# Performance work log

Hardware: AMD Instinct MI355X
Metric: run time of the kernel (lower is better)

The kernel has to match this reference:

```python
import jax, jax.numpy as jnp
import numpy as np

TAU = 1.0  # initial_temperature, non-trainable
EPS = 1e-10


def setup_inputs() -> dict:
    key = jax.random.key(0)
    ks = jax.random.split(key, 5)
    B, D, E, A = 8192, 1024, 32, 128
    x = jax.random.normal(ks[0], (B, D), dtype=jnp.float32)
    W_att = jax.random.normal(ks[1], (E, D), dtype=jnp.float32) * (1.0 / np.sqrt(D))
    b_att = jnp.zeros((E,), dtype=jnp.float32)
    adaptive_bias = jnp.zeros((E,), dtype=jnp.float32)
    W_strat = jax.random.normal(ks[2], (E, A, D), dtype=jnp.float32) * (1.0 / np.sqrt(D))
    b_strat = jnp.zeros((E, A), dtype=jnp.float32)
    gumbel_u = jax.random.uniform(ks[3], (B, E), dtype=jnp.float32)
    return {"x": x, "W_att": W_att, "b_att": b_att, "adaptive_bias": adaptive_bias,
            "W_strat": W_strat, "b_strat": b_strat, "gumbel_u": gumbel_u}


def reference(x, W_att, b_att, adaptive_bias, W_strat, b_strat, gumbel_u):
    # Gating: linear + adaptive bias, then gumbel-softmax with temperature TAU
    logits = x @ W_att.T + b_att + adaptive_bias            # [B, E]
    g = -jnp.log(-jnp.log(gumbel_u + EPS) + EPS)            # gumbel noise [B, E]
    weights = jax.nn.softmax((logits + g) / TAU, axis=-1)   # [B, E] soft selection
    # Per-strategy outputs: each strategy is Linear(D -> A)
    strat_out = jnp.einsum('bd,ead->bea', x, W_strat) + b_strat  # [B, E, A]
    # Weighted combine (superposition)
    out = jnp.einsum('be,bea->ba', weights, strat_out)      # [B, A]
    return out
```

## Files before the change

kernel.cpp:

```cpp
#include <hip/hip_runtime.h>
#include <stdint.h>

typedef unsigned short u16;
typedef __attribute__((ext_vector_type(4))) float f32x4;
typedef __attribute__((ext_vector_type(8))) short short8;
typedef __attribute__((ext_vector_type(8))) unsigned short u16x8;

static constexpr int Bq = 8192;
static constexpr int Dq = 1024;
static constexpr int Eq = 32;
static constexpr int Aq = 128;
static constexpr int NSTRAT = 4096;

__device__ inline u16 f32_to_bf16_rne(float f) {
    uint32_t u = __float_as_uint(f);
    uint32_t r = 0x7fffu + ((u >> 16) & 1u);
    return (u16)((u + r) >> 16);
}
__device__ inline float bf16_to_f32(u16 h) {
    return __uint_as_float(((uint32_t)h) << 16);
}
__device__ inline void gload_lds16(const u16* g, u16* l) {
    __builtin_amdgcn_global_load_lds(
        (const __attribute__((address_space(1))) void*)g,
        (__attribute__((address_space(3))) void*)l, 16, 0, 0);
}

__global__ __launch_bounds__(256) void cvt_x_kernel(const float* __restrict__ src,
                                                    u16* __restrict__ dst) {
    size_t i = ((size_t)blockIdx.x * 256 + threadIdx.x) * 8;
    f32x4 a = *(const f32x4*)(src + i);
    f32x4 b = *(const f32x4*)(src + i + 4);
    u16x8 o;
    o[0] = f32_to_bf16_rne(a[0]); o[1] = f32_to_bf16_rne(a[1]);
    o[2] = f32_to_bf16_rne(a[2]); o[3] = f32_to_bf16_rne(a[3]);
    o[4] = f32_to_bf16_rne(b[0]); o[5] = f32_to_bf16_rne(b[1]);
    o[6] = f32_to_bf16_rne(b[2]); o[7] = f32_to_bf16_rne(b[3]);
    *(u16x8*)(dst + i) = o;
}

__global__ __launch_bounds__(256) void cvt_w_kernel(const float* __restrict__ src,
                                                    u16* __restrict__ dst) {
    size_t i = ((size_t)blockIdx.x * 256 + threadIdx.x) * 8;
    f32x4 a = *(const f32x4*)(src + i);
    f32x4 b = *(const f32x4*)(src + i + 4);
    u16x8 o;
    o[0] = f32_to_bf16_rne(a[0]); o[1] = f32_to_bf16_rne(a[1]);
    o[2] = f32_to_bf16_rne(a[2]); o[3] = f32_to_bf16_rne(a[3]);
    o[4] = f32_to_bf16_rne(b[0]); o[5] = f32_to_bf16_rne(b[1]);
    o[6] = f32_to_bf16_rne(b[2]); o[7] = f32_to_bf16_rne(b[3]);
    *(u16x8*)(dst + i) = o;
}

#define FBAR do { asm volatile("" ::: "memory"); __builtin_amdgcn_s_barrier(); asm volatile("" ::: "memory"); } while (0)
#define LGKM0 asm volatile("s_waitcnt lgkmcnt(0)" ::: "memory")
#define VMCNT(n) asm volatile("s_waitcnt vmcnt(" #n ")" ::: "memory")
#define SB __builtin_amdgcn_sched_barrier(0)
#define PRIO1 __builtin_amdgcn_s_setprio(1)
#define PRIO0 __builtin_amdgcn_s_setprio(0)
#define MF(a, b, c) __builtin_amdgcn_mfma_f32_16x16x32_bf16(a, b, c, 0, 0, 0)


#define STAGE_A(buf, h, kt) do { \
    gload_lds16(agA + (size_t)((h)*128) * 1024 + (size_t)(kt) * 64, (u16*)&lds[buf][h][tid * 8]); \
    gload_lds16(agA + (size_t)((h)*128 + 64) * 1024 + (size_t)(kt) * 64, (u16*)&lds[buf][h][4096 + tid * 8]); \
} while (0)
#define STAGE_B(buf, h, kt) do { \
    gload_lds16(agB + (size_t)((h)*128) * 1024 + (size_t)(kt) * 64, (u16*)&lds[buf][2 + (h)][tid * 8]); \
    gload_lds16(agB + (size_t)((h)*128 + 64) * 1024 + (size_t)(kt) * 64, (u16*)&lds[buf][2 + (h)][4096 + tid * 8]); \
} while (0)

#define LDA8(DST, ABASE, mq) do { \
    DST[0] = *(const short8*)((ABASE) + (mq)*4096 + 0*1024 + aoff0); \
    DST[1] = *(const short8*)((ABASE) + (mq)*4096 + 0*1024 + aoff1); \
    DST[2] = *(const short8*)((ABASE) + (mq)*4096 + 1*1024 + aoff0); \
    DST[3] = *(const short8*)((ABASE) + (mq)*4096 + 1*1024 + aoff1); \
    DST[4] = *(const short8*)((ABASE) + (mq)*4096 + 2*1024 + aoff0); \
    DST[5] = *(const short8*)((ABASE) + (mq)*4096 + 2*1024 + aoff1); \
    DST[6] = *(const short8*)((ABASE) + (mq)*4096 + 3*1024 + aoff0); \
    DST[7] = *(const short8*)((ABASE) + (mq)*4096 + 3*1024 + aoff1); \
} while (0)
#define LDB4(DST, BBASE, nq) do { \
    DST[0] = *(const short8*)((BBASE) + (nq)*2048 + 0*1024 + boff0); \
    DST[1] = *(const short8*)((BBASE) + (nq)*2048 + 0*1024 + boff1); \
    DST[2] = *(const short8*)((BBASE) + (nq)*2048 + 1*1024 + boff0); \
    DST[3] = *(const short8*)((BBASE) + (nq)*2048 + 1*1024 + boff1); \
} while (0)

#define QUAD(mq, nq, AS, BS) do { \
    acc[(mq)*4+0][(nq)*2+0] = MF(AS[0], BS[0], acc[(mq)*4+0][(nq)*2+0]); \
    acc[(mq)*4+0][(nq)*2+1] = MF(AS[0], BS[2], acc[(mq)*4+0][(nq)*2+1]); \
    acc[(mq)*4+1][(nq)*2+0] = MF(AS[2], BS[0], acc[(mq)*4+1][(nq)*2+0]); \
    acc[(mq)*4+1][(nq)*2+1] = MF(AS[2], BS[2], acc[(mq)*4+1][(nq)*2+1]); \
    acc[(mq)*4+2][(nq)*2+0] = MF(AS[4], BS[0], acc[(mq)*4+2][(nq)*2+0]); \
    acc[(mq)*4+2][(nq)*2+1] = MF(AS[4], BS[2], acc[(mq)*4+2][(nq)*2+1]); \
    acc[(mq)*4+3][(nq)*2+0] = MF(AS[6], BS[0], acc[(mq)*4+3][(nq)*2+0]); \
    acc[(mq)*4+3][(nq)*2+1] = MF(AS[6], BS[2], acc[(mq)*4+3][(nq)*2+1]); \
    acc[(mq)*4+0][(nq)*2+0] = MF(AS[1], BS[1], acc[(mq)*4+0][(nq)*2+0]); \
    acc[(mq)*4+0][(nq)*2+1] = MF(AS[1], BS[3], acc[(mq)*4+0][(nq)*2+1]); \
    acc[(mq)*4+1][(nq)*2+0] = MF(AS[3], BS[1], acc[(mq)*4+1][(nq)*2+0]); \
    acc[(mq)*4+1][(nq)*2+1] = MF(AS[3], BS[3], acc[(mq)*4+1][(nq)*2+1]); \
    acc[(mq)*4+2][(nq)*2+0] = MF(AS[5], BS[1], acc[(mq)*4+2][(nq)*2+0]); \
    acc[(mq)*4+2][(nq)*2+1] = MF(AS[5], BS[3], acc[(mq)*4+2][(nq)*2+1]); \
    acc[(mq)*4+3][(nq)*2+0] = MF(AS[7], BS[1], acc[(mq)*4+3][(nq)*2+0]); \
    acc[(mq)*4+3][(nq)*2+1] = MF(AS[7], BS[3], acc[(mq)*4+3][(nq)*2+1]); \
} while (0)

#define GITER(t, TAIL) do { \
     \
    LDB4(Bs0, Bbase0, 0); \
    STAGE_A(1, 0, (t) + 1); \
    SB; FBAR; LGKM0; SB; \
    PRIO1; QUAD(0, 0, As0, Bs0); PRIO0; SB; FBAR; \
     \
    LDB4(Bs1, Bbase0, 1); \
    STAGE_A(1, 1, (t) + 1); \
    SB; FBAR; LGKM0; SB; \
    PRIO1; QUAD(0, 1, As0, Bs1); PRIO0; SB; FBAR; \
     \
    LDA8(As1, Abase0, 1); \
    if (!(TAIL)) STAGE_B(0, 0, (t) + 2); \
    SB; FBAR; LGKM0; SB; \
    PRIO1; QUAD(1, 1, As1, Bs1); PRIO0; SB; \
    if (TAIL) { VMCNT(0); } else { VMCNT(2); } \
    FBAR; \
     \
    LDA8(As0, Abase1, 0); \
    if (!(TAIL)) STAGE_B(0, 1, (t) + 2); \
    SB; FBAR; LGKM0; SB; \
    PRIO1; QUAD(1, 0, As1, Bs0); PRIO0; SB; FBAR; \
     \
    LDB4(Bs0, Bbase1, 0); \
    if (!(TAIL)) STAGE_A(0, 0, (t) + 2); \
    SB; FBAR; LGKM0; SB; \
    PRIO1; QUAD(0, 0, As0, Bs0); PRIO0; SB; FBAR; \
     \
    LDB4(Bs1, Bbase1, 1); \
    if (!(TAIL)) STAGE_A(0, 1, (t) + 2); \
    SB; FBAR; LGKM0; SB; \
    PRIO1; QUAD(0, 1, As0, Bs1); PRIO0; SB; FBAR; \
     \
    LDA8(As1, Abase1, 1); \
    if (!(TAIL)) STAGE_B(1, 0, (t) + 3); \
    SB; FBAR; LGKM0; SB; \
    PRIO1; QUAD(1, 1, As1, Bs1); PRIO0; SB; \
    if (!(TAIL)) { VMCNT(2); } \
    FBAR; \
     \
    if (!(TAIL)) { LDA8(As0, Abase0, 0); STAGE_B(1, 1, (t) + 3); } \
    SB; FBAR; LGKM0; SB; \
    PRIO1; QUAD(1, 0, As1, Bs0); PRIO0; SB; FBAR; \
} while (0)

__global__ __launch_bounds__(512, 2) void gemm256(const u16* __restrict__ Abuf,
                                                  const u16* __restrict__ Bbuf,
                                                  u16* __restrict__ S) {
    __shared__ __align__(16) u16 lds[2][4][8192];

    const int tid = threadIdx.x;
    const int lane = tid & 63;
    const int wv = tid >> 6;
    const int wr = wv >> 2;
    const int wc = wv & 3;
    const int fr = lane & 15;
    const int fq = lane >> 4;

    const int bid = blockIdx.x;
    const int swz = (bid & 7) * 64 + (bid >> 3);
    const int m0 = (swz >> 4) * 256;
    const int n0 = (swz & 15) * 256;

    const int s_r = tid >> 3;
    const int s_c = ((tid & 7) * 8) ^ ((s_r & 7) << 3);
    const u16* agA = Abuf + (size_t)(m0 + s_r) * 1024 + s_c;
    const u16* agB = Bbuf + (size_t)(n0 + s_r) * 1024 + s_c;

    const int aoff0 = fr * 64 + ((fq ^ (fr & 7)) * 8);
    const int aoff1 = fr * 64 + (((fq + 4) ^ (fr & 7)) * 8);
    const int bof = (wc & 1) * 4096;
    const int boff0 = bof + aoff0;
    const int boff1 = bof + aoff1;

    const u16* Abase0 = (const u16*)&lds[0][wr][0];
    const u16* Abase1 = (const u16*)&lds[1][wr][0];
    const u16* Bbase0 = (const u16*)&lds[0][2 + (wc >> 1)][0];
    const u16* Bbase1 = (const u16*)&lds[1][2 + (wc >> 1)][0];

    f32x4 acc[8][4] = {};
    short8 As0[8], As1[8], Bs0[4], Bs1[4];

    STAGE_A(0, 0, 0); STAGE_A(0, 1, 0); STAGE_B(0, 0, 0); STAGE_B(0, 1, 0);
    STAGE_B(1, 0, 1); STAGE_B(1, 1, 1);
    SB; VMCNT(4); FBAR;
    LDA8(As0, Abase0, 0);

#pragma unroll 1
    for (int t = 0; t < 14; t += 2) { GITER(t, 0); }
    GITER(14, 1);

    const int crow = m0 + wr * 128 + fq * 4;
    const int ccol = n0 + wc * 64 + fr;
#pragma unroll
    for (int im = 0; im < 8; ++im)
#pragma unroll
        for (int jn = 0; jn < 4; ++jn)
#pragma unroll
            for (int q = 0; q < 4; ++q)
                S[(size_t)(crow + im * 16 + q) * NSTRAT + ccol + jn * 16] =
                    f32_to_bf16_rne(acc[im][jn][q]);
}

__global__ __launch_bounds__(512) void logits_kernel(const u16* __restrict__ xb,
                                                     const float* __restrict__ W_att,
                                                     const float* __restrict__ b_att,
                                                     const float* __restrict__ abias,
                                                     const float* __restrict__ gu,
                                                     float* __restrict__ w) {
    __shared__ __align__(16) u16 Wa[32][1032];

    const int tid = threadIdx.x;
    const int lane = tid & 63;
    const int wv = tid >> 6;
    const int fr = lane & 15;
    const int fq = lane >> 4;
    const int m0 = blockIdx.x * 128;

    {
        const int row = tid >> 4;
        const int col0 = (tid & 15) * 64;
        const float* src = W_att + (size_t)row * 1024 + col0;
        u16* dst = &Wa[row][col0];
#pragma unroll
        for (int it = 0; it < 8; ++it) {
            f32x4 a = *(const f32x4*)(src + it * 8);
            f32x4 b = *(const f32x4*)(src + it * 8 + 4);
            u16x8 o;
            o[0] = f32_to_bf16_rne(a[0]); o[1] = f32_to_bf16_rne(a[1]);
            o[2] = f32_to_bf16_rne(a[2]); o[3] = f32_to_bf16_rne(a[3]);
            o[4] = f32_to_bf16_rne(b[0]); o[5] = f32_to_bf16_rne(b[1]);
            o[6] = f32_to_bf16_rne(b[2]); o[7] = f32_to_bf16_rne(b[3]);
            *(u16x8*)(dst + it * 8) = o;
        }
    }
    __syncthreads();

    f32x4 acc0 = {}, acc1 = {};
    const u16* xrow = xb + (size_t)(m0 + wv * 16 + fr) * 1024 + fq * 8;
#pragma unroll 4
    for (int k0 = 0; k0 < 1024; k0 += 32) {
        short8 a0 = *(const short8*)(xrow + k0);
        short8 b0 = *(const short8*)(&Wa[fr][k0 + fq * 8]);
        short8 b1 = *(const short8*)(&Wa[16 + fr][k0 + fq * 8]);
        acc0 = MF(a0, b0, acc0);
        acc1 = MF(a0, b1, acc1);
    }

    const float bba0 = b_att[fr] + abias[fr];
    const float bba1 = b_att[16 + fr] + abias[16 + fr];
#pragma unroll
    for (int q = 0; q < 4; ++q) {
        const int row = m0 + wv * 16 + fq * 4 + q;
        float u0 = gu[(size_t)row * 32 + fr];
        float u1 = gu[(size_t)row * 32 + 16 + fr];
        float g0 = -logf(-logf(u0 + 1e-10f) + 1e-10f);
        float g1 = -logf(-logf(u1 + 1e-10f) + 1e-10f);
        float z0 = acc0[q] + bba0 + g0;
        float z1 = acc1[q] + bba1 + g1;
        float mx = fmaxf(z0, z1);
#pragma unroll
        for (int s = 1; s < 16; s <<= 1) mx = fmaxf(mx, __shfl_xor(mx, s));
        float p0 = __expf(z0 - mx);
        float p1 = __expf(z1 - mx);
        float sm = p0 + p1;
#pragma unroll
        for (int s = 1; s < 16; s <<= 1) sm += __shfl_xor(sm, s);
        float inv = 1.0f / sm;
        w[(size_t)row * 32 + fr] = p0 * inv;
        w[(size_t)row * 32 + 16 + fr] = p1 * inv;
    }
}

__global__ __launch_bounds__(256) void combine_kernel(const u16* __restrict__ S,
                                                      const float* __restrict__ w,
                                                      const float* __restrict__ b_strat,
                                                      float* __restrict__ out) {
    int b = blockIdx.x * 2 + (threadIdx.x >> 7);
    int a = threadIdx.x & 127;
    const u16* Srow = S + (size_t)b * NSTRAT;
    const float* wrow = w + (size_t)b * 32;
    float acc = 0.f;
#pragma unroll
    for (int e = 0; e < 32; ++e) {
        acc += wrow[e] * (bf16_to_f32(Srow[e * 128 + a]) + b_strat[e * 128 + a]);
    }
    out[(size_t)b * 128 + a] = acc;
}

extern "C" void kernel_launch(void* const* d_in, const int* in_sizes, int n_in,
                              void* d_out, int out_size, void* d_ws, size_t ws_size,
                              hipStream_t stream) {
    (void)in_sizes; (void)n_in; (void)out_size; (void)ws_size;
    const float* x       = (const float*)d_in[0];
    const float* W_att   = (const float*)d_in[1];
    const float* b_att   = (const float*)d_in[2];
    const float* abias   = (const float*)d_in[3];
    const float* W_strat = (const float*)d_in[4];
    const float* b_strat = (const float*)d_in[5];
    const float* gu      = (const float*)d_in[6];
    float* out = (float*)d_out;

    u16* xb = (u16*)d_ws;
    u16* Wb = xb + (size_t)Bq * Dq;
    u16* S  = Wb + (size_t)NSTRAT * Dq;
    float* w = (float*)(S + (size_t)Bq * NSTRAT);

    cvt_x_kernel<<<(Bq * Dq) / (256 * 8), 256, 0, stream>>>(x, xb);
    cvt_w_kernel<<<(NSTRAT * Dq) / (256 * 8), 256, 0, stream>>>(W_strat, Wb);

    logits_kernel<<<Bq / 128, 512, 0, stream>>>(xb, W_att, b_att, abias, gu, w);

    gemm256<<<512, 512, 0, stream>>>(xb, Wb, S);

    combine_kernel<<<Bq / 2, 256, 0, stream>>>(S, w, b_strat, out);
}
```

Measured before the change: 108.7 us.

## Fuse weighted combine into GEMM epilogue via atomics, merge conversion kernels

The GEMM epilogue no longer writes the bf16 strategy-output matrix S. It multiplies each accumulator by the gating weight for its expert and atomically adds the product into the output, which is pre-initialised with the weighted bias sum. This removes a 64MB write plus the read in the combine kernel. It adds fp32 atomics, with 32 experts contending per output element, and makes the summation order nondeterministic. The two conversion kernels are also merged into one launch.

```diff
diff --git a/kernel.cpp b/kernel.cpp
--- a/kernel.cpp
+++ b/kernel.cpp
@@ -26,30 +26,20 @@
         (__attribute__((address_space(3))) void*)l, 16, 0, 0);
 }
 
-__global__ __launch_bounds__(256) void cvt_x_kernel(const float* __restrict__ src,
-                                                    u16* __restrict__ dst) {
+__global__ __launch_bounds__(256) void cvt_fused(const float* __restrict__ x,
+                                                 const float* __restrict__ Ws,
+                                                 u16* __restrict__ xb) {
     size_t i = ((size_t)blockIdx.x * 256 + threadIdx.x) * 8;
-    f32x4 a = *(const f32x4*)(src + i);
-    f32x4 b = *(const f32x4*)(src + i + 4);
+    const size_t XN = (size_t)Bq * Dq;
+    const float* src = (i < XN) ? (x + i) : (Ws + (i - XN));
+    f32x4 a = *(const f32x4*)(src);
+    f32x4 b = *(const f32x4*)(src + 4);
     u16x8 o;
     o[0] = f32_to_bf16_rne(a[0]); o[1] = f32_to_bf16_rne(a[1]);
     o[2] = f32_to_bf16_rne(a[2]); o[3] = f32_to_bf16_rne(a[3]);
     o[4] = f32_to_bf16_rne(b[0]); o[5] = f32_to_bf16_rne(b[1]);
     o[6] = f32_to_bf16_rne(b[2]); o[7] = f32_to_bf16_rne(b[3]);
-    *(u16x8*)(dst + i) = o;
-}
-
-__global__ __launch_bounds__(256) void cvt_w_kernel(const float* __restrict__ src,
-                                                    u16* __restrict__ dst) {
-    size_t i = ((size_t)blockIdx.x * 256 + threadIdx.x) * 8;
-    f32x4 a = *(const f32x4*)(src + i);
-    f32x4 b = *(const f32x4*)(src + i + 4);
-    u16x8 o;
-    o[0] = f32_to_bf16_rne(a[0]); o[1] = f32_to_bf16_rne(a[1]);
-    o[2] = f32_to_bf16_rne(a[2]); o[3] = f32_to_bf16_rne(a[3]);
-    o[4] = f32_to_bf16_rne(b[0]); o[5] = f32_to_bf16_rne(b[1]);
-    o[6] = f32_to_bf16_rne(b[2]); o[7] = f32_to_bf16_rne(b[3]);
-    *(u16x8*)(dst + i) = o;
+    *(u16x8*)(xb + i) = o;
 }
 
 #define FBAR do { asm volatile("" ::: "memory"); __builtin_amdgcn_s_barrier(); asm volatile("" ::: "memory"); } while (0)
@@ -154,7 +144,8 @@
 
 __global__ __launch_bounds__(512, 2) void gemm256(const u16* __restrict__ Abuf,
                                                   const u16* __restrict__ Bbuf,
-                                                  u16* __restrict__ S) {
+                                                  const float* __restrict__ w,
+                                                  float* __restrict__ out) {
     __shared__ __align__(16) u16 lds[2][4][8192];
 
     const int tid = threadIdx.x;
@@ -199,15 +190,20 @@
     GITER(14, 1);
 
     const int crow = m0 + wr * 128 + fq * 4;
-    const int ccol = n0 + wc * 64 + fr;
-#pragma unroll
-    for (int im = 0; im < 8; ++im)
-#pragma unroll
-        for (int jn = 0; jn < 4; ++jn)
-#pragma unroll
-            for (int q = 0; q < 4; ++q)
-                S[(size_t)(crow + im * 16 + q) * NSTRAT + ccol + jn * 16] =
-                    f32_to_bf16_rne(acc[im][jn][q]);
+    const int e = (n0 >> 7) + (wc >> 1);
+    const int abase = (wc & 1) * 64 + fr;
+#pragma unroll
+    for (int im = 0; im < 8; ++im) {
+#pragma unroll
+        for (int q = 0; q < 4; ++q) {
+            const int row = crow + im * 16 + q;
+            const float wv_ = w[(size_t)row * 32 + e];
+            float* orow = out + (size_t)row * 128 + abase;
+#pragma unroll
+            for (int jn = 0; jn < 4; ++jn)
+                atomicAdd(orow + jn * 16, wv_ * acc[im][jn][q]);
+        }
+    }
 }
 
 __global__ __launch_bounds__(512) void logits_kernel(const u16* __restrict__ xb,
@@ -280,19 +276,16 @@
     }
 }
 
-__global__ __launch_bounds__(256) void combine_kernel(const u16* __restrict__ S,
-                                                      const float* __restrict__ w,
-                                                      const float* __restrict__ b_strat,
-                                                      float* __restrict__ out) {
+__global__ __launch_bounds__(256) void init_out_kernel(const float* __restrict__ w,
+                                                       const float* __restrict__ b_strat,
+                                                       float* __restrict__ out) {
     int b = blockIdx.x * 2 + (threadIdx.x >> 7);
     int a = threadIdx.x & 127;
-    const u16* Srow = S + (size_t)b * NSTRAT;
     const float* wrow = w + (size_t)b * 32;
     float acc = 0.f;
 #pragma unroll
-    for (int e = 0; e < 32; ++e) {
-        acc += wrow[e] * (bf16_to_f32(Srow[e * 128 + a]) + b_strat[e * 128 + a]);
-    }
+    for (int e = 0; e < 32; ++e)
+        acc += wrow[e] * b_strat[e * 128 + a];
     out[(size_t)b * 128 + a] = acc;
 }
 
@@ -311,15 +304,13 @@
 
     u16* xb = (u16*)d_ws;
     u16* Wb = xb + (size_t)Bq * Dq;
-    u16* S  = Wb + (size_t)NSTRAT * Dq;
-    float* w = (float*)(S + (size_t)Bq * NSTRAT);
-
-    cvt_x_kernel<<<(Bq * Dq) / (256 * 8), 256, 0, stream>>>(x, xb);
-    cvt_w_kernel<<<(NSTRAT * Dq) / (256 * 8), 256, 0, stream>>>(W_strat, Wb);
+    float* w = (float*)(Wb + (size_t)NSTRAT * Dq);
+
+    cvt_fused<<<(Bq * Dq + NSTRAT * Dq) / (256 * 8), 256, 0, stream>>>(x, W_strat, xb);
 
     logits_kernel<<<Bq / 128, 512, 0, stream>>>(xb, W_att, b_att, abias, gu, w);
 
-    gemm256<<<512, 512, 0, stream>>>(xb, Wb, S);
-
-    combine_kernel<<<Bq / 2, 256, 0, stream>>>(S, w, b_strat, out);
-}
+    init_out_kernel<<<Bq / 2, 256, 0, stream>>>(w, b_strat, out);
+
+    gemm256<<<512, 512, 0, stream>>>(xb, Wb, w, out);
+}
```

Result: slower. 204.9 us (+88.5%).
